# Performance work log

Hardware: AMD Instinct MI355X
Metric: run time of the kernel (lower is better)

The kernel has to match this reference:

```python
import jax, jax.numpy as jnp
import numpy as np

K = 3
STRIDE = 1
PAD = 1
DIL = 1


def setup_inputs() -> dict:
    key = jax.random.key(0)
    k1, k2, k3, k4 = jax.random.split(key, 4)
    B, C, H, W = 8, 256, 64, 64
    Cout = 256
    x = jax.random.normal(k1, (B, C, H, W), jnp.float32)
    # offsets in units of pixels; keep them modest like a trained DCN
    offset = jax.random.normal(k2, (B, 2 * K * K, H, W), jnp.float32)
    weight = jax.random.normal(k3, (Cout, C, K, K), jnp.float32) * 0.02
    bias = jax.random.normal(k4, (Cout,), jnp.float32) * 0.02
    return {"x": x, "offset": offset, "weight": weight, "bias": bias}


def _deform_conv(x, offset, weight, bias):
    B, C, H, W = x.shape
    Ho = (H + 2 * PAD - DIL * (K - 1) - 1) // STRIDE + 1
    Wo = (W + 2 * PAD - DIL * (K - 1) - 1) // STRIDE + 1
    KK = K * K

    # base sampling grid per kernel tap: [KK, Ho, Wo] via broadcasting
    ky, kx = jnp.meshgrid(jnp.arange(K), jnp.arange(K), indexing="ij")
    base_y = (jnp.arange(Ho) * STRIDE - PAD)[None, :, None] + (ky.reshape(-1) * DIL)[:, None, None]
    base_x = (jnp.arange(Wo) * STRIDE - PAD)[None, None, :] + (kx.reshape(-1) * DIL)[:, None, None]

    # offset layout (dg=1): [B, KK, 2, Ho, Wo], (y, x) per tap
    off = offset.reshape(B, KK, 2, Ho, Wo)
    py = base_y[None].astype(x.dtype) + off[:, :, 0]  # [B, KK, Ho, Wo]
    px = base_x[None].astype(x.dtype) + off[:, :, 1]

    y0f = jnp.floor(py)
    x0f = jnp.floor(px)
    wy = (py - y0f).reshape(B, 1, -1)  # [B, 1, KK*Ho*Wo]
    wx = (px - x0f).reshape(B, 1, -1)
    y0 = y0f.astype(jnp.int32)
    x0 = x0f.astype(jnp.int32)

    x_flat = x.reshape(B, C, H * W)

    def corner(yi, xi):
        # zero-padded bilinear corner gather -> [B, C, KK*Ho*Wo]
        valid = ((yi >= 0) & (yi < H) & (xi >= 0) & (xi < W)).reshape(B, 1, -1)
        yc = jnp.clip(yi, 0, H - 1)
        xc = jnp.clip(xi, 0, W - 1)
        idx = (yc * W + xc).reshape(B, -1)
        g = jax.vmap(lambda img, i: img[:, i])(x_flat, idx)
        return g * valid.astype(x.dtype)

    v00 = corner(y0, x0)
    v01 = corner(y0, x0 + 1)
    v10 = corner(y0 + 1, x0)
    v11 = corner(y0 + 1, x0 + 1)

    val = (v00 * (1 - wy) * (1 - wx) + v01 * (1 - wy) * wx
           + v10 * wy * (1 - wx) + v11 * wy * wx)  # [B, C, KK*Ho*Wo]

    # im2col columns: [B, C*KK, Ho*Wo] with (Cin outer, tap inner) matching weight flatten
    cols = val.reshape(B, C, KK, Ho * Wo).reshape(B, C * KK, Ho * Wo)
    W2 = weight.reshape(weight.shape[0], -1)  # [Cout, Cin*KK]
    out = jnp.einsum("on,bnp->bop", W2, cols) + bias[None, :, None]
    return out.reshape(B, -1, Ho, Wo)


def reference(x, offset, weight, bias):
    return _deform_conv(x, offset, weight, bias)
```

## Files before the change

kernel.cpp:

```cpp
#include <hip/hip_runtime.h>
#include <cstdint>
#include <cstddef>


#define B_   8
#define C_   256
#define H_   64
#define W_   64
#define CO_  256
#define KK_  9

typedef short  short8   __attribute__((ext_vector_type(8)));
typedef float  f32x4    __attribute__((ext_vector_type(4)));
typedef float  f32x2    __attribute__((ext_vector_type(2)));

__device__ inline short f2bf(float f) {
    uint32_t u = __builtin_bit_cast(uint32_t, f);
    u += 0x7FFFu + ((u >> 16) & 1u);
    return (short)(u >> 16);
}
__device__ inline float bf2f(short s) {
    return __builtin_bit_cast(float, (uint32_t)(uint16_t)s << 16);
}

__global__ __launch_bounds__(256) void wperm_frag(const float* __restrict__ w,
                                                  short* __restrict__ wp) {
    const int i = blockIdx.x * 256 + threadIdx.x;
    const int lane_w = i & 63;
    const int rest   = i >> 6;
    const int kk     = rest % 9;
    const int rest2  = rest / 9;
    const int ch     = rest2 & 7;
    const int cofrag = rest2 >> 3;
    const int co     = cofrag * 16 + (lane_w & 15);
    const int cb     = ch * 32 + (lane_w >> 4) * 8;
    short8 v;
#pragma unroll
    for (int j = 0; j < 8; ++j)
        v[j] = f2bf(w[((size_t)co * C_ + cb + j) * KK_ + kk]);
    *reinterpret_cast<short8*>(wp + (size_t)i * 8) = v;
}

__global__ __launch_bounds__(256) void xpose(const float* __restrict__ x,
                                             short* __restrict__ xT) {
    __shared__ short tile[64 * 258];
    const int bid = blockIdx.x;
    const int y = bid & 63;
    const int b = bid >> 6;
    const int t = threadIdx.x;
    const int c4 = t >> 6;
    const int xw = t & 63;
    const float* src = x + (size_t)b * (C_ * H_ * W_) + (size_t)y * W_ + xw;
#pragma unroll 8
    for (int j = 0; j < 64; ++j) {
        const int c = j * 4 + c4;
        tile[xw * 258 + c] = f2bf(src[(size_t)c * (H_ * W_)]);
    }
    __syncthreads();
    short* dst = xT + ((size_t)(b * (H_ * W_)) + y * W_) * C_;
#pragma unroll
    for (int r = 0; r < 8; ++r) {
        const int idx = r * 256 + t;
        const int xw2 = idx >> 5;
        const int c2  = (idx & 31) * 8;
        *reinterpret_cast<short8*>(dst + xw2 * C_ + c2) =
            *reinterpret_cast<const short8*>(&tile[xw2 * 258 + c2]);
    }
}

__global__ __launch_bounds__(1024, 8) void dcn_mfma6(
    const short* __restrict__ xT,
    const float* __restrict__ offset,
    const short* __restrict__ wfr,
    const float* __restrict__ bias,
    float* __restrict__ out)
{
    __shared__ uint32_t t_pA[KK_ * 64];
    __shared__ uint32_t t_pB[KK_ * 64];
    __shared__ f32x4    t_wv[KK_ * 64];
    __shared__ short    colsF[4 * 9 * 512];

    const int bid = blockIdx.x;
    const int b   = bid & 7;
    const int ho  = bid >> 3;

    const int t    = threadIdx.x;
    const int lane = t & 63;
    const int wave = t >> 6;

    if (t < KK_ * 64) {
        const int e  = t;
        const int kk = e >> 6;
        const int wo = e & 63;
        const int ky = kk / 3, kx = kk % 3;
        const float offy = offset[(((b * 18) + kk * 2 + 0) * 64 + ho) * 64 + wo];
        const float offx = offset[(((b * 18) + kk * 2 + 1) * 64 + ho) * 64 + wo];
        const float py  = (float)(ho - 1 + ky) + offy;
        const float pxx = (float)(wo - 1 + kx) + offx;
        const float y0f = floorf(py), x0f = floorf(pxx);
        const float wy = py - y0f, wx = pxx - x0f;
        const int y0 = (int)y0f, x0 = (int)x0f;
        const int y1 = y0 + 1,   x1 = x0 + 1;
        const float vy0 = (y0 >= 0 && y0 < H_) ? 1.f : 0.f;
        const float vy1 = (y1 >= 0 && y1 < H_) ? 1.f : 0.f;
        const float vx0 = (x0 >= 0 && x0 < W_) ? 1.f : 0.f;
        const float vx1 = (x1 >= 0 && x1 < W_) ? 1.f : 0.f;
        f32x4 wv;
        wv[0] = (1.f - wy) * (1.f - wx) * vy0 * vx0;
        wv[1] = (1.f - wy) * wx         * vy0 * vx1;
        wv[2] = wy         * (1.f - wx) * vy1 * vx0;
        wv[3] = wy         * wx         * vy1 * vx1;
        const int y0c = min(max(y0, 0), H_ - 1);
        const int y1c = min(max(y1, 0), H_ - 1);
        const int x0c = min(max(x0, 0), W_ - 1);
        const int x1c = min(max(x1, 0), W_ - 1);
        t_pA[e] = (uint32_t)(y0c * W_ + x0c) | ((uint32_t)(y0c * W_ + x1c) << 16);
        t_pB[e] = (uint32_t)(y1c * W_ + x0c) | ((uint32_t)(y1c * W_ + x1c) << 16);
        t_wv[e] = wv;
    }
    __syncthreads();

    f32x4 acc00 = (f32x4)0.f, acc01 = (f32x4)0.f;
    f32x4 acc10 = (f32x4)0.f, acc11 = (f32x4)0.f;

    const int cog = wave >> 1;
    const int pxg = wave & 1;
    const int m_l = lane & 15;

    const short* af0b = wfr + ((size_t)(cog * 2 + 0) * 8) * 9 * 512 + lane * 8;
    const short* af1b = wfr + ((size_t)(cog * 2 + 1) * 8) * 9 * 512 + lane * 8;
    const short* bf0b = &colsF[((pxg * 2 + 0) * 9) * 512 + lane * 8];
    const short* bf1b = &colsF[((pxg * 2 + 1) * 9) * 512 + lane * 8];

    const int soct = t & 3;
    const int spx  = (t >> 2) & 63;
    const int srep = t >> 8;
    const char* xq = (const char*)xT + ((size_t)b << 21) + soct * 16;
    short* const cw_base = &colsF[((spx >> 4) * 9) * 512 + ((spx & 15) + (soct << 4)) * 8];

    for (int ch = 0; ch < 8; ++ch) {
        const char* xc = xq + ch * 64;
#pragma unroll
        for (int jj = 0; jj < 3; ++jj) {
            const int kk = srep + jj * 4;
            if (kk < KK_) {
                const int e  = kk * 64 + spx;
                const uint32_t pA = t_pA[e];
                const uint32_t pB = t_pB[e];
                const f32x4    wv = t_wv[e];
                short8 s00, s01, s10, s11;
                __builtin_memcpy(&s00, xc + (size_t)(pA & 0xFFFFu) * 512, 16);
                __builtin_memcpy(&s01, xc + (size_t)(pA >> 16)     * 512, 16);
                __builtin_memcpy(&s10, xc + (size_t)(pB & 0xFFFFu) * 512, 16);
                __builtin_memcpy(&s11, xc + (size_t)(pB >> 16)     * 512, 16);
                short8 vs;
#pragma unroll
                for (int j = 0; j < 8; ++j) {
                    const float v = wv[0] * bf2f(s00[j]) + wv[1] * bf2f(s01[j])
                                  + wv[2] * bf2f(s10[j]) + wv[3] * bf2f(s11[j]);
                    vs[j] = f2bf(v);
                }
                *reinterpret_cast<short8*>(cw_base + kk * 512) = vs;
            }
        }
        __syncthreads();

        const short* a0 = af0b + (size_t)ch * 9 * 512;
        const short* a1 = af1b + (size_t)ch * 9 * 512;
#pragma unroll
        for (int kk = 0; kk < 9; ++kk) {
            short8 af0, af1, bf0, bf1;
            __builtin_memcpy(&af0, a0 + kk * 512, 16);
            __builtin_memcpy(&af1, a1 + kk * 512, 16);
            __builtin_memcpy(&bf0, bf0b + kk * 512, 16);
            __builtin_memcpy(&bf1, bf1b + kk * 512, 16);
            acc00 = __builtin_amdgcn_mfma_f32_16x16x32_bf16(af0, bf0, acc00, 0, 0, 0);
            acc01 = __builtin_amdgcn_mfma_f32_16x16x32_bf16(af0, bf1, acc01, 0, 0, 0);
            acc10 = __builtin_amdgcn_mfma_f32_16x16x32_bf16(af1, bf0, acc10, 0, 0, 0);
            acc11 = __builtin_amdgcn_mfma_f32_16x16x32_bf16(af1, bf1, acc11, 0, 0, 0);
        }
        __syncthreads();
    }

    const int r0 = (lane >> 4) << 2;
    const int co_b = cog * 32;
    const int px_b = pxg * 32;
#pragma unroll
    for (int r = 0; r < 4; ++r) {
        {
            const int co = co_b + r0 + r;
            const float bv = bias[co];
            float* orow = out + ((size_t)(b * CO_ + co) * H_ + ho) * W_;
            orow[px_b + m_l]      = acc00[r] + bv;
            orow[px_b + 16 + m_l] = acc01[r] + bv;
        }
        {
            const int co = co_b + 16 + r0 + r;
            const float bv = bias[co];
            float* orow = out + ((size_t)(b * CO_ + co) * H_ + ho) * W_;
            orow[px_b + m_l]      = acc10[r] + bv;
            orow[px_b + 16 + m_l] = acc11[r] + bv;
        }
    }
}

#define PADK 296
__global__ __launch_bounds__(256) void w2bf_fb(const float* __restrict__ w,
                                               short* __restrict__ wb, int n8) {
    const int i = blockIdx.x * 256 + threadIdx.x;
    if (i >= n8) return;
    const f32x4 a = *reinterpret_cast<const f32x4*>(w + (size_t)i * 8);
    const f32x4 bq = *reinterpret_cast<const f32x4*>(w + (size_t)i * 8 + 4);
    short8 v;
#pragma unroll
    for (int j = 0; j < 4; ++j) { v[j] = f2bf(a[j]); v[j + 4] = f2bf(bq[j]); }
    *reinterpret_cast<short8*>(wb + (size_t)i * 8) = v;
}

__global__ __launch_bounds__(512, 2) void dcn_mfma_fb(
    const float* __restrict__ x,
    const float* __restrict__ offset,
    const short* __restrict__ wbf,
    const float* __restrict__ bias,
    float* __restrict__ out)
{
    __shared__ uint32_t t_oab[KK_ * 64];
    __shared__ f32x4    t_wv[KK_ * 64];
    __shared__ short    colsf[64 * PADK];

    const int bid = blockIdx.x;
    const int ho  = bid & 63;
    const int b   = bid >> 6;
    const int t    = threadIdx.x;
    const int lane = t & 63;
    const int wave = t >> 6;

    for (int e = t; e < KK_ * 64; e += 512) {
        const int kk = e >> 6;
        const int wo = e & 63;
        const int ky = kk / 3, kx = kk % 3;
        const float offy = offset[(((b * 18) + kk * 2 + 0) * 64 + ho) * 64 + wo];
        const float offx = offset[(((b * 18) + kk * 2 + 1) * 64 + ho) * 64 + wo];
        const float py  = (float)(ho - 1 + ky) + offy;
        const float pxx = (float)(wo - 1 + kx) + offx;
        const float y0f = floorf(py), x0f = floorf(pxx);
        const float wy = py - y0f, wx = pxx - x0f;
        const int y0 = (int)y0f, x0 = (int)x0f;
        const int y1 = y0 + 1,   x1 = x0 + 1;
        const float vy0 = (y0 >= 0 && y0 < H_) ? 1.f : 0.f;
        const float vy1 = (y1 >= 0 && y1 < H_) ? 1.f : 0.f;
        const float vx0 = (x0 >= 0 && x0 < W_) ? 1.f : 0.f;
        const float vx1 = (x1 >= 0 && x1 < W_) ? 1.f : 0.f;
        const float wv0 = (1.f - wy) * (1.f - wx) * vy0 * vx0;
        const float wv1 = (1.f - wy) * wx         * vy0 * vx1;
        const float wv2 = wy         * (1.f - wx) * vy1 * vx0;
        const float wv3 = wy         * wx         * vy1 * vx1;
        const int y0c = min(max(y0, 0), H_ - 1);
        const int y1c = min(max(y1, 0), H_ - 1);
        const int x0c = min(max(x0, 0), W_ - 1);
        const int x1c = min(max(x1, 0), W_ - 1);
        const int pb  = min(max(x0, 0), W_ - 2);
        const float sA0 = (x0c == pb)     ? 1.f : 0.f;
        const float sB0 = (x1c == pb)     ? 1.f : 0.f;
        const float sA1 = (x0c == pb + 1) ? 1.f : 0.f;
        const float sB1 = (x1c == pb + 1) ? 1.f : 0.f;
        f32x4 wv;
        wv[0] = sA0 * wv0 + sB0 * wv1;
        wv[1] = sA1 * wv0 + sB1 * wv1;
        wv[2] = sA0 * wv2 + sB0 * wv3;
        wv[3] = sA1 * wv2 + sB1 * wv3;
        t_oab[e] = (uint32_t)((y0c * W_ + pb) * 4) |
                   ((uint32_t)((y1c * W_ + pb) * 4) << 16);
        t_wv[e] = wv;
    }
    __syncthreads();

    f32x4 acc[4][2];
#pragma unroll
    for (int i = 0; i < 4; ++i) { acc[i][0] = (f32x4)0.f; acc[i][1] = (f32x4)0.f; }

    const int wm = wave >> 1;
    const int wn = wave & 1;
    const int co0 = __builtin_amdgcn_readfirstlane(wm * 64);
    const int px0 = __builtin_amdgcn_readfirstlane(wn * 32);
    const int wqs = __builtin_amdgcn_readfirstlane(wave);
    const int m_l = lane & 15;
    const int k_l = (lane >> 4) << 3;

    const short* wrow[4];
#pragma unroll
    for (int mt = 0; mt < 4; ++mt)
        wrow[mt] = wbf + (size_t)(co0 + mt * 16 + m_l) * (C_ * KK_);

    for (int c0 = 0; c0 < C_; c0 += 32) {
        const char* xp[4];
#pragma unroll
        for (int dc = 0; dc < 4; ++dc)
            xp[dc] = (const char*)(x + ((size_t)(b * C_ + c0 + 4 * wqs + dc) << 12));
#pragma unroll
        for (int j = 0; j < 9; ++j) {
            short vs[4];
#pragma unroll
            for (int jj = 0; jj < 4; ++jj) {
                const int idx = j * 4 + jj;
                const int dc  = idx / 9;
                const int kk  = idx % 9;
                const uint32_t oab = t_oab[kk * 64 + lane];
                const f32x4    wv  = t_wv[kk * 64 + lane];
                f32x2 lo, hi;
                __builtin_memcpy(&lo, xp[dc] + (oab & 0xFFFFu), 8);
                __builtin_memcpy(&hi, xp[dc] + (oab >> 16), 8);
                vs[jj] = f2bf(wv[0] * lo[0] + wv[1] * lo[1] +
                              wv[2] * hi[0] + wv[3] * hi[1]);
            }
            short* cw = &colsf[lane * PADK + (wave * 9 + j) * 4];
            cw[0] = vs[0]; cw[1] = vs[1]; cw[2] = vs[2]; cw[3] = vs[3];
        }
        __syncthreads();
#pragma unroll
        for (int s = 0; s < 9; ++s) {
            const int krow = s * 32 + k_l;
            const short8 bfA = *reinterpret_cast<const short8*>(
                &colsf[(px0 + m_l) * PADK + krow]);
            const short8 bfB = *reinterpret_cast<const short8*>(
                &colsf[(px0 + 16 + m_l) * PADK + krow]);
            const int kglob = c0 * 9 + krow;
#pragma unroll
            for (int mt = 0; mt < 4; ++mt) {
                const short8 af = *reinterpret_cast<const short8*>(wrow[mt] + kglob);
                acc[mt][0] = __builtin_amdgcn_mfma_f32_16x16x32_bf16(
                    af, bfA, acc[mt][0], 0, 0, 0);
                acc[mt][1] = __builtin_amdgcn_mfma_f32_16x16x32_bf16(
                    af, bfB, acc[mt][1], 0, 0, 0);
            }
        }
        __syncthreads();
    }

    const int r0 = (lane >> 4) << 2;
#pragma unroll
    for (int mt = 0; mt < 4; ++mt) {
#pragma unroll
        for (int r = 0; r < 4; ++r) {
            const int co = co0 + mt * 16 + r0 + r;
            const float bv = bias[co];
            float* orow = out + ((size_t)(b * CO_ + co) * H_ + ho) * W_;
            orow[px0 + m_l]      = acc[mt][0][r] + bv;
            orow[px0 + 16 + m_l] = acc[mt][1][r] + bv;
        }
    }
}

extern "C" void kernel_launch(void* const* d_in, const int* in_sizes, int n_in,
                              void* d_out, int out_size, void* d_ws, size_t ws_size,
                              hipStream_t stream) {
    const float* x      = (const float*)d_in[0];
    const float* offset = (const float*)d_in[1];
    const float* weight = (const float*)d_in[2];
    const float* bias   = (const float*)d_in[3];
    float* out = (float*)d_out;
    (void)in_sizes; (void)n_in; (void)out_size;

    const size_t WPM_BYTES = (size_t)CO_ * C_ * KK_ * 2;
    const size_t XT_BYTES  = (size_t)B_ * H_ * W_ * C_ * 2;

    if (ws_size >= WPM_BYTES + XT_BYTES) {
        short* wfr = (short*)d_ws;
        short* xT  = (short*)((char*)d_ws + WPM_BYTES);
        hipLaunchKernelGGL(wperm_frag, dim3(288), dim3(256), 0, stream, weight, wfr);
        hipLaunchKernelGGL(xpose,      dim3(512), dim3(256), 0, stream, x, xT);
        hipLaunchKernelGGL(dcn_mfma6,  dim3(512), dim3(1024), 0, stream,
                           xT, offset, wfr, bias, out);
    } else {
        short* wbf = (short*)d_ws;
        hipLaunchKernelGGL(w2bf_fb, dim3(288), dim3(256), 0, stream,
                           weight, wbf, 73728);
        hipLaunchKernelGGL(dcn_mfma_fb, dim3(512), dim3(512), 0, stream,
                           x, offset, wbf, bias, out);
    }
}
```

Measured before the change: 86.88 us.

## Double-buffer the im2col LDS tile and pack sampling tables compactly

The bilinear gather for the next channel chunk now runs before the MFMA loop on the current chunk, using two LDS column buffers. This drops one barrier per iteration and lets gather latency overlap with matrix work. The per-tap tables also shrink: corner coordinates are packed into one word and the four bilinear weights are stored as bf16 pairs. That lowers LDS footprint and read traffic, at the cost of rounding the interpolation weights to bf16.

```diff
diff --git a/kernel.cpp b/kernel.cpp
--- a/kernel.cpp
+++ b/kernel.cpp
@@ -9,10 +9,10 @@
 #define W_   64
 #define CO_  256
 #define KK_  9
-
-typedef short  short8   __attribute__((ext_vector_type(8)));
-typedef float  f32x4    __attribute__((ext_vector_type(4)));
-typedef float  f32x2    __attribute__((ext_vector_type(2)));
+#define BUFSZ (4 * 9 * 512)
+
+typedef short    short8 __attribute__((ext_vector_type(8)));
+typedef float    f32x4  __attribute__((ext_vector_type(4)));
 
 __device__ inline short f2bf(float f) {
     uint32_t u = __builtin_bit_cast(uint32_t, f);
@@ -21,6 +21,12 @@
 }
 __device__ inline float bf2f(short s) {
     return __builtin_bit_cast(float, (uint32_t)(uint16_t)s << 16);
+}
+__device__ inline float lof(uint32_t u) {
+    return __builtin_bit_cast(float, u << 16);
+}
+__device__ inline float hif(uint32_t u) {
+    return __builtin_bit_cast(float, u & 0xFFFF0000u);
 }
 
 __global__ __launch_bounds__(256) void wperm_frag(const float* __restrict__ w,
@@ -68,17 +74,17 @@
     }
 }
 
-__global__ __launch_bounds__(1024, 8) void dcn_mfma6(
+__global__ __launch_bounds__(1024, 8) void dcn_mfma9(
     const short* __restrict__ xT,
     const float* __restrict__ offset,
     const short* __restrict__ wfr,
     const float* __restrict__ bias,
     float* __restrict__ out)
 {
-    __shared__ uint32_t t_pA[KK_ * 64];
-    __shared__ uint32_t t_pB[KK_ * 64];
-    __shared__ f32x4    t_wv[KK_ * 64];
-    __shared__ short    colsF[4 * 9 * 512];
+    __shared__ uint32_t t_cp [KK_ * 64];
+    __shared__ uint32_t t_w01[KK_ * 64];
+    __shared__ uint32_t t_w23[KK_ * 64];
+    __shared__ short    colsF[2][BUFSZ];
 
     const int bid = blockIdx.x;
     const int b   = bid & 7;
@@ -105,18 +111,20 @@
         const float vy1 = (y1 >= 0 && y1 < H_) ? 1.f : 0.f;
         const float vx0 = (x0 >= 0 && x0 < W_) ? 1.f : 0.f;
         const float vx1 = (x1 >= 0 && x1 < W_) ? 1.f : 0.f;
-        f32x4 wv;
-        wv[0] = (1.f - wy) * (1.f - wx) * vy0 * vx0;
-        wv[1] = (1.f - wy) * wx         * vy0 * vx1;
-        wv[2] = wy         * (1.f - wx) * vy1 * vx0;
-        wv[3] = wy         * wx         * vy1 * vx1;
+        const float wv0 = (1.f - wy) * (1.f - wx) * vy0 * vx0;
+        const float wv1 = (1.f - wy) * wx         * vy0 * vx1;
+        const float wv2 = wy         * (1.f - wx) * vy1 * vx0;
+        const float wv3 = wy         * wx         * vy1 * vx1;
         const int y0c = min(max(y0, 0), H_ - 1);
         const int y1c = min(max(y1, 0), H_ - 1);
         const int x0c = min(max(x0, 0), W_ - 1);
         const int x1c = min(max(x1, 0), W_ - 1);
-        t_pA[e] = (uint32_t)(y0c * W_ + x0c) | ((uint32_t)(y0c * W_ + x1c) << 16);
-        t_pB[e] = (uint32_t)(y1c * W_ + x0c) | ((uint32_t)(y1c * W_ + x1c) << 16);
-        t_wv[e] = wv;
+        t_cp[e]  = (uint32_t)x0c | ((uint32_t)y0c << 6)
+                 | ((uint32_t)x1c << 12) | ((uint32_t)y1c << 18);
+        t_w01[e] = (uint32_t)(uint16_t)f2bf(wv0)
+                 | ((uint32_t)(uint16_t)f2bf(wv1) << 16);
+        t_w23[e] = (uint32_t)(uint16_t)f2bf(wv2)
+                 | ((uint32_t)(uint16_t)f2bf(wv3) << 16);
     }
     __syncthreads();
 
@@ -129,42 +137,58 @@
 
     const short* af0b = wfr + ((size_t)(cog * 2 + 0) * 8) * 9 * 512 + lane * 8;
     const short* af1b = wfr + ((size_t)(cog * 2 + 1) * 8) * 9 * 512 + lane * 8;
-    const short* bf0b = &colsF[((pxg * 2 + 0) * 9) * 512 + lane * 8];
-    const short* bf1b = &colsF[((pxg * 2 + 1) * 9) * 512 + lane * 8];
+    const int bfo0 = ((pxg * 2 + 0) * 9) * 512 + lane * 8;
+    const int bfo1 = ((pxg * 2 + 1) * 9) * 512 + lane * 8;
 
     const int soct = t & 3;
     const int spx  = (t >> 2) & 63;
     const int srep = t >> 8;
-    const char* xq = (const char*)xT + ((size_t)b << 21) + soct * 16;
-    short* const cw_base = &colsF[((spx >> 4) * 9) * 512 + ((spx & 15) + (soct << 4)) * 8];
+    const uint32_t socto = (uint32_t)(soct * 16);
+    const char* xbase = (const char*)xT + ((size_t)b << 21);
+    const int cwo = ((spx >> 4) * 9) * 512 + ((spx & 15) + (soct << 4)) * 8;
+    const int e0 = srep * 64 + spx;
+    const int e1 = (srep + 4) * 64 + spx;
+    const int e2 = 8 * 64 + spx;
+    const int kk0v = srep;
+    const int kk1v = srep + 4;
+
+#define GTASK(EIDX, KKI, XC, DBUF) { \
+    const uint32_t cp  = t_cp[EIDX]; \
+    const uint32_t w01 = t_w01[EIDX]; \
+    const uint32_t w23 = t_w23[EIDX]; \
+    const uint32_t q00 = ((cp & 0xFFFu) << 9) + socto; \
+    const uint32_t q01 = (((cp & 0xFC0u) | ((cp >> 12) & 63u)) << 9) + socto; \
+    const uint32_t q10 = (((((cp >> 12) & 0xFC0u)) | (cp & 63u)) << 9) + socto; \
+    const uint32_t q11 = (((cp >> 12) & 0xFFFu) << 9) + socto; \
+    short8 s00, s01, s10, s11; \
+    __builtin_memcpy(&s00, (XC) + q00, 16); \
+    __builtin_memcpy(&s01, (XC) + q01, 16); \
+    __builtin_memcpy(&s10, (XC) + q10, 16); \
+    __builtin_memcpy(&s11, (XC) + q11, 16); \
+    const float wv0 = lof(w01), wv1 = hif(w01); \
+    const float wv2 = lof(w23), wv3 = hif(w23); \
+    short8 vs; \
+    _Pragma("unroll") \
+    for (int j = 0; j < 8; ++j) { \
+        const float v = wv0 * bf2f(s00[j]) + wv1 * bf2f(s01[j]) \
+                      + wv2 * bf2f(s10[j]) + wv3 * bf2f(s11[j]); \
+        vs[j] = f2bf(v); \
+    } \
+    *reinterpret_cast<short8*>(&(DBUF)[cwo + (KKI) * 512]) = vs; }
+
+#define STAGE(CI, DBUF) { \
+    const char* xci = xbase + (CI) * 64; \
+    GTASK(e0, kk0v, xci, DBUF) \
+    GTASK(e1, kk1v, xci, DBUF) \
+    if (srep == 0) { GTASK(e2, 8, xci, DBUF) } }
+
+    STAGE(0, colsF[0])
+    __syncthreads();
 
     for (int ch = 0; ch < 8; ++ch) {
-        const char* xc = xq + ch * 64;
-#pragma unroll
-        for (int jj = 0; jj < 3; ++jj) {
-            const int kk = srep + jj * 4;
-            if (kk < KK_) {
-                const int e  = kk * 64 + spx;
-                const uint32_t pA = t_pA[e];
-                const uint32_t pB = t_pB[e];
-                const f32x4    wv = t_wv[e];
-                short8 s00, s01, s10, s11;
-                __builtin_memcpy(&s00, xc + (size_t)(pA & 0xFFFFu) * 512, 16);
-                __builtin_memcpy(&s01, xc + (size_t)(pA >> 16)     * 512, 16);
-                __builtin_memcpy(&s10, xc + (size_t)(pB & 0xFFFFu) * 512, 16);
-                __builtin_memcpy(&s11, xc + (size_t)(pB >> 16)     * 512, 16);
-                short8 vs;
-#pragma unroll
-                for (int j = 0; j < 8; ++j) {
-                    const float v = wv[0] * bf2f(s00[j]) + wv[1] * bf2f(s01[j])
-                                  + wv[2] * bf2f(s10[j]) + wv[3] * bf2f(s11[j]);
-                    vs[j] = f2bf(v);
-                }
-                *reinterpret_cast<short8*>(cw_base + kk * 512) = vs;
-            }
-        }
-        __syncthreads();
-
+        if (ch < 7) { STAGE(ch + 1, colsF[(ch + 1) & 1]) }
+
+        const short* bufr = &colsF[ch & 1][0];
         const short* a0 = af0b + (size_t)ch * 9 * 512;
         const short* a1 = af1b + (size_t)ch * 9 * 512;
 #pragma unroll
@@ -172,8 +196,8 @@
             short8 af0, af1, bf0, bf1;
             __builtin_memcpy(&af0, a0 + kk * 512, 16);
             __builtin_memcpy(&af1, a1 + kk * 512, 16);
-            __builtin_memcpy(&bf0, bf0b + kk * 512, 16);
-            __builtin_memcpy(&bf1, bf1b + kk * 512, 16);
+            __builtin_memcpy(&bf0, bufr + bfo0 + kk * 512, 16);
+            __builtin_memcpy(&bf1, bufr + bfo1 + kk * 512, 16);
             acc00 = __builtin_amdgcn_mfma_f32_16x16x32_bf16(af0, bf0, acc00, 0, 0, 0);
             acc01 = __builtin_amdgcn_mfma_f32_16x16x32_bf16(af0, bf1, acc01, 0, 0, 0);
             acc10 = __builtin_amdgcn_mfma_f32_16x16x32_bf16(af1, bf0, acc10, 0, 0, 0);
@@ -181,6 +205,8 @@
         }
         __syncthreads();
     }
+#undef STAGE
+#undef GTASK
 
     const int r0 = (lane >> 4) << 2;
     const int co_b = cog * 32;
@@ -307,11 +333,11 @@
                 const int kk  = idx % 9;
                 const uint32_t oab = t_oab[kk * 64 + lane];
                 const f32x4    wv  = t_wv[kk * 64 + lane];
-                f32x2 lo, hi;
+                struct { float a, b; } lo, hi;
                 __builtin_memcpy(&lo, xp[dc] + (oab & 0xFFFFu), 8);
                 __builtin_memcpy(&hi, xp[dc] + (oab >> 16), 8);
-                vs[jj] = f2bf(wv[0] * lo[0] + wv[1] * lo[1] +
-                              wv[2] * hi[0] + wv[3] * hi[1]);
+                vs[jj] = f2bf(wv[0] * lo.a + wv[1] * lo.b +
+                              wv[2] * hi.a + wv[3] * hi.b);
             }
             short* cw = &colsf[lane * PADK + (wave * 9 + j) * 4];
             cw[0] = vs[0]; cw[1] = vs[1]; cw[2] = vs[2]; cw[3] = vs[3];
@@ -369,7 +395,7 @@
         short* xT  = (short*)((char*)d_ws + WPM_BYTES);
         hipLaunchKernelGGL(wperm_frag, dim3(288), dim3(256), 0, stream, weight, wfr);
         hipLaunchKernelGGL(xpose,      dim3(512), dim3(256), 0, stream, x, xT);
-        hipLaunchKernelGGL(dcn_mfma6,  dim3(512), dim3(1024), 0, stream,
+        hipLaunchKernelGGL(dcn_mfma9,  dim3(512), dim3(1024), 0, stream,
                            xT, offset, wfr, bias, out);
     } else {
         short* wbf = (short*)d_ws;
```

Result: no change. 87.05 us (+0.2%).
